# Performance work log

Measured on AMD Instinct MI355X. Metric: run time of the kernel, lower is better.

Reference implementation:

```python
import jax, jax.numpy as jnp
import numpy as np

N = 100000
E = 1600000
F_IN, H, C = 128, 128, 64


def setup_inputs() -> dict:
    key = jax.random.key(0)
    ks = jax.random.split(key, 8)
    x = jax.random.normal(ks[0], (N, F_IN), dtype=jnp.float32)
    edge_index = jax.random.randint(ks[1], (2, E), 0, N, dtype=jnp.int64)
    s = lambda fi: (1.0 / np.sqrt(fi))
    # SAGEConv1: lin_l (applied to mean-aggregated neighbors, has bias), lin_r (root, no bias)
    W1l = jax.random.uniform(ks[2], (H, F_IN), jnp.float32, -s(F_IN), s(F_IN))
    b1 = jnp.zeros((H,), jnp.float32)
    W1r = jax.random.uniform(ks[3], (H, F_IN), jnp.float32, -s(F_IN), s(F_IN))
    # SAGEConv2
    W2l = jax.random.uniform(ks[4], (C, H), jnp.float32, -s(H), s(H))
    b2 = jnp.zeros((C,), jnp.float32)
    W2r = jax.random.uniform(ks[5], (C, H), jnp.float32, -s(H), s(H))
    return {"x": x, "edge_index": edge_index, "W1l": W1l, "b1": b1, "W1r": W1r,
            "W2l": W2l, "b2": b2, "W2r": W2r}


def _mean_aggr(x, src, dst):
    # mean over incoming neighbors (PyG flow: edge_index[0]=source -> edge_index[1]=target)
    msg = x[src]                                            # [E, F] big gather
    summed = jax.ops.segment_sum(msg, dst, num_segments=N)  # [N, F]
    cnt = jax.ops.segment_sum(jnp.ones((src.shape[0],), x.dtype), dst, num_segments=N)
    return summed / jnp.clip(cnt, 1.0)[:, None]


def _sage_conv(x, src, dst, Wl, b, Wr):
    agg = _mean_aggr(x, src, dst)
    return agg @ Wl.T + b + x @ Wr.T


def _iconv(x, src, dst):
    # weight-free GCN propagation: D^-1/2 (A + I) D^-1/2 @ x
    loops = jnp.arange(N, dtype=src.dtype)
    s2 = jnp.concatenate([src, loops])
    d2 = jnp.concatenate([dst, loops])
    deg = jax.ops.segment_sum(jnp.ones((s2.shape[0],), x.dtype), d2, num_segments=N)
    dis = jnp.where(deg > 0, jax.lax.rsqrt(jnp.maximum(deg, 1.0)), 0.0)
    norm = dis[s2] * dis[d2]                               # [E+N]
    return jax.ops.segment_sum(norm[:, None] * x[s2], d2, num_segments=N)


def reference(x, edge_index, W1l, b1, W1r, W2l, b2, W2r):
    src, dst = edge_index[0], edge_index[1]
    h = jax.nn.relu(_sage_conv(x, src, dst, W1l, b1, W1r))
    # F.dropout(training=False) -> identity in eval mode
    h = _sage_conv(h, src, dst, W2l, b2, W2r)
    return _iconv(h, src, dst)
```

## Files before the change

kernel.cpp:

```cpp
#include <hip/hip_runtime.h>

#define GN 100000
#define GE 1600000
#define GF 128
#define GH 128
#define GC 64

#define NB 392
#define SLABSZ 5376
#define P1_EDGES 4096
#define P1_BLOCKS ((GE + P1_EDGES - 1) / P1_EDGES)
#define CASTX_BLOCKS 12500

typedef __attribute__((ext_vector_type(8))) short v8s;
typedef __attribute__((ext_vector_type(4))) float v4f;

__device__ __forceinline__ unsigned short f2bf(float f) {
    union { float f; unsigned u; } a; a.f = f;
    unsigned r = a.u + 0x7fff + ((a.u >> 16) & 1);
    return (unsigned short)(r >> 16);
}
__device__ __forceinline__ float bf2f(unsigned short b) {
    union { unsigned u; float f; } a; a.u = ((unsigned)b) << 16;
    return a.f;
}

__global__ __launch_bounds__(256) void prep_kernel(
    unsigned* __restrict__ slab, int* __restrict__ bucket_cnt,
    const int* __restrict__ src, const int* __restrict__ dst,
    unsigned short* __restrict__ xb, const float* __restrict__ x,
    unsigned short* w1l, unsigned short* w1r,
    unsigned short* w2l, unsigned short* w2r,
    const float* W1l, const float* W1r,
    const float* W2l, const float* W2r)
{
    __shared__ int hist[512];
    __shared__ int scanex[512];
    __shared__ int cursor[512];
    __shared__ int gbase[512];
    __shared__ int ssum[256];
    __shared__ unsigned stage[P1_EDGES];
    __shared__ unsigned short sbid[P1_EDGES];

    int tid = threadIdx.x;
    int blk = blockIdx.x;

    if (blk >= P1_BLOCKS) {
        int cb = blk - P1_BLOCKS;
        if (cb < CASTX_BLOCKS) {
            int i = cb * 256 + tid;
            float4 v = ((const float4*)x)[i];
            ushort4 u;
            u.x = f2bf(v.x); u.y = f2bf(v.y); u.z = f2bf(v.z); u.w = f2bf(v.w);
            ((ushort4*)xb)[i] = u;
            return;
        }
        int i = (cb - CASTX_BLOCKS) * 256 + tid;
        const float* s; unsigned short* d; int off;
        if      (i <  4096) { s = W1l; d = w1l; off = i; }
        else if (i <  8192) { s = W1r; d = w1r; off = i - 4096; }
        else if (i < 10240) { s = W2l; d = w2l; off = i - 8192; }
        else if (i < 12288) { s = W2r; d = w2r; off = i - 10240; }
        else return;
        float4 v = ((const float4*)s)[off];
        ushort4 u;
        u.x = f2bf(v.x); u.y = f2bf(v.y); u.z = f2bf(v.z); u.w = f2bf(v.w);
        ((ushort4*)d)[off] = u;
        return;
    }

    int e0 = blk * P1_EDGES;
    int nE = min(P1_EDGES, GE - e0);

    unsigned pk[16]; int bk[16];
    hist[tid] = 0; hist[tid + 256] = 0;
    __syncthreads();
    #pragma unroll
    for (int j = 0; j < 16; ++j) {
        int i = j * 256 + tid;
        if (i < nE) {
            int e = e0 + i;
            int d = dst[e], s = src[e];
            int b = d >> 8;
            pk[j] = ((unsigned)(d & 255) << 17) | (unsigned)s;
            bk[j] = b;
            atomicAdd(&hist[b], 1);
        } else bk[j] = -1;
    }
    __syncthreads();
    int a0 = hist[2 * tid], a1 = hist[2 * tid + 1];
    int s2 = a0 + a1;
    ssum[tid] = s2;
    __syncthreads();
    for (int off = 1; off < 256; off <<= 1) {
        int v = (tid >= off) ? ssum[tid - off] : 0;
        __syncthreads();
        ssum[tid] += v;
        __syncthreads();
    }
    int pbase = ssum[tid] - s2;
    scanex[2 * tid] = pbase;          cursor[2 * tid] = pbase;
    scanex[2 * tid + 1] = pbase + a0; cursor[2 * tid + 1] = pbase + a0;
    __syncthreads();
    #pragma unroll
    for (int j = 0; j < 16; ++j) {
        if (bk[j] >= 0) {
            int pos = atomicAdd(&cursor[bk[j]], 1);
            stage[pos] = pk[j];
            sbid[pos] = (unsigned short)bk[j];
        }
    }
    for (int b = tid; b < NB; b += 256) {
        int c = hist[b];
        gbase[b] = c ? atomicAdd(&bucket_cnt[b], c) : 0;
    }
    __syncthreads();
    for (int i = tid; i < nE; i += 256) {
        int b = sbid[i];
        int go = gbase[b] + (i - scanex[b]);
        if (go < SLABSZ)
            slab[(size_t)b * SLABSZ + go] = stage[i];
    }
}

__global__ __launch_bounds__(256) void bucket_pass2_kernel(
    int* __restrict__ csr, int* __restrict__ row_ptr,
    float* __restrict__ invc, float* __restrict__ dis,
    const unsigned* __restrict__ slab, const int* __restrict__ bucket_cnt)
{
    __shared__ int deg_l[256];
    __shared__ int excl[256];
    __shared__ int cur[256];
    __shared__ int ssum[256];
    __shared__ int bstart_s;
    __shared__ unsigned stage[SLABSZ];

    int t = threadIdx.x;
    int b = blockIdx.x;

    int c0 = (2 * t < NB) ? bucket_cnt[2 * t] : 0;
    int c1 = (2 * t + 1 < NB) ? bucket_cnt[2 * t + 1] : 0;
    int sc = c0 + c1;
    ssum[t] = sc;
    __syncthreads();
    for (int off = 1; off < 256; off <<= 1) {
        int v = (t >= off) ? ssum[t - off] : 0;
        __syncthreads();
        ssum[t] += v;
        __syncthreads();
    }
    int pb = ssum[t] - sc;
    if (2 * t == b)     bstart_s = pb;
    if (2 * t + 1 == b) bstart_s = pb + c0;
    if (b == NB - 1 && t == 0) row_ptr[GN] = GE;

    int cnt = min(bucket_cnt[b], SLABSZ);
    const unsigned* sp = slab + (size_t)b * SLABSZ;
    deg_l[t] = 0;
    __syncthreads();
    int base = bstart_s;
    for (int i = t; i < cnt; i += 256)
        atomicAdd(&deg_l[sp[i] >> 17], 1);
    __syncthreads();
    int dg = deg_l[t];
    ssum[t] = dg;
    __syncthreads();
    for (int off = 1; off < 256; off <<= 1) {
        int v = (t >= off) ? ssum[t - off] : 0;
        __syncthreads();
        ssum[t] += v;
        __syncthreads();
    }
    int ex = ssum[t] - dg;
    excl[t] = ex; cur[t] = ex;
    __syncthreads();
    int d = b * 256 + t;
    if (d < GN) {
        row_ptr[d] = base + ex;
        float c = (float)dg;
        invc[d] = 1.0f / fmaxf(c, 1.0f);
        dis[d] = rsqrtf(c + 1.0f);
    }
    for (int i = t; i < cnt; i += 256) {
        unsigned p = sp[i];
        int pos = atomicAdd(&cur[p >> 17], 1);
        stage[pos] = p & 0x1FFFFu;
    }
    __syncthreads();
    for (int i = t; i < cnt; i += 256)
        csr[base + i] = (int)stage[i];
}

__global__ __launch_bounds__(256) void fused_gemm_kernel(
    unsigned short* __restrict__ P, unsigned short* __restrict__ Q,
    const unsigned short* __restrict__ A1, const unsigned short* __restrict__ A2,
    const unsigned short* __restrict__ W1, const unsigned short* __restrict__ W2,
    const unsigned short* __restrict__ Wl, const unsigned short* __restrict__ Wr,
    const float* __restrict__ b1, const float* __restrict__ b2, int M)
{
    __shared__ unsigned short hs[256][136];

    int tid = threadIdx.x;
    int wv = tid >> 6, lane = tid & 63;
    int lm = lane & 15, quad = lane >> 4;
    int m_base = blockIdx.x * 256 + wv * 64;
    int row_l0 = wv * 64;

    for (int nh = 0; nh < 2; ++nh) {
        int n_base = nh * 64;
        v4f acc[4][4];
        #pragma unroll
        for (int mt = 0; mt < 4; ++mt)
            #pragma unroll
            for (int nt = 0; nt < 4; ++nt) acc[mt][nt] = (v4f){0.f,0.f,0.f,0.f};

        #pragma unroll
        for (int ks = 0; ks < 4; ++ks) {
            int koff = ks * 32 + quad * 8;
            v8s a1[4], a2[4], bw1[4], bw2[4];
            #pragma unroll
            for (int mt = 0; mt < 4; ++mt) {
                int row = m_base + mt * 16 + lm;
                if (row < M) {
                    a1[mt] = *(const v8s*)(A1 + (size_t)row * 128 + koff);
                    a2[mt] = *(const v8s*)(A2 + (size_t)row * 128 + koff);
                } else {
                    a1[mt] = (v8s){0,0,0,0,0,0,0,0};
                    a2[mt] = (v8s){0,0,0,0,0,0,0,0};
                }
            }
            #pragma unroll
            for (int nt = 0; nt < 4; ++nt) {
                int col = n_base + nt * 16 + lm;
                bw1[nt] = *(const v8s*)(W1 + (size_t)col * 128 + koff);
                bw2[nt] = *(const v8s*)(W2 + (size_t)col * 128 + koff);
            }
            #pragma unroll
            for (int mt = 0; mt < 4; ++mt)
                #pragma unroll
                for (int nt = 0; nt < 4; ++nt) {
                    acc[mt][nt] = __builtin_amdgcn_mfma_f32_16x16x32_bf16(a1[mt], bw1[nt], acc[mt][nt], 0, 0, 0);
                    acc[mt][nt] = __builtin_amdgcn_mfma_f32_16x16x32_bf16(a2[mt], bw2[nt], acc[mt][nt], 0, 0, 0);
                }
        }

        #pragma unroll
        for (int mt = 0; mt < 4; ++mt)
            #pragma unroll
            for (int r = 0; r < 4; ++r) {
                int rl = row_l0 + mt * 16 + quad * 4 + r;
                #pragma unroll
                for (int nt = 0; nt < 4; ++nt) {
                    int col = n_base + nt * 16 + lm;
                    float v = acc[mt][nt][r] + b1[col];
                    hs[rl][col] = f2bf(fmaxf(v, 0.f));
                }
            }
    }
    __syncthreads();

    v4f accP[4][4], accQ[4][4];
    #pragma unroll
    for (int mt = 0; mt < 4; ++mt)
        #pragma unroll
        for (int nt = 0; nt < 4; ++nt) {
            accP[mt][nt] = (v4f){0.f,0.f,0.f,0.f};
            accQ[mt][nt] = (v4f){0.f,0.f,0.f,0.f};
        }

    #pragma unroll
    for (int ks = 0; ks < 4; ++ks) {
        int koff = ks * 32 + quad * 8;
        v8s af[4], bl[4], br[4];
        #pragma unroll
        for (int mt = 0; mt < 4; ++mt)
            af[mt] = *(const v8s*)&hs[row_l0 + mt * 16 + lm][koff];
        #pragma unroll
        for (int nt = 0; nt < 4; ++nt) {
            int col = nt * 16 + lm;
            bl[nt] = *(const v8s*)(Wl + (size_t)col * 128 + koff);
            br[nt] = *(const v8s*)(Wr + (size_t)col * 128 + koff);
        }
        #pragma unroll
        for (int mt = 0; mt < 4; ++mt)
            #pragma unroll
            for (int nt = 0; nt < 4; ++nt) {
                accP[mt][nt] = __builtin_amdgcn_mfma_f32_16x16x32_bf16(af[mt], bl[nt], accP[mt][nt], 0, 0, 0);
                accQ[mt][nt] = __builtin_amdgcn_mfma_f32_16x16x32_bf16(af[mt], br[nt], accQ[mt][nt], 0, 0, 0);
            }
    }

    #pragma unroll
    for (int mt = 0; mt < 4; ++mt)
        #pragma unroll
        for (int r = 0; r < 4; ++r) {
            int row = m_base + mt * 16 + quad * 4 + r;
            if (row >= M) continue;
            #pragma unroll
            for (int nt = 0; nt < 4; ++nt) {
                int col = nt * 16 + lm;
                P[(size_t)row * 64 + col] = f2bf(accP[mt][nt][r]);
                Q[(size_t)row * 64 + col] = f2bf(accQ[mt][nt][r] + b2[col]);
            }
        }
}

__global__ __launch_bounds__(256) void gather_mean128_kernel(
    unsigned short* __restrict__ out, const unsigned short* __restrict__ in,
    const float* __restrict__ invc, const int* __restrict__ row_ptr,
    const int* __restrict__ csr, int N)
{
    int wid = (blockIdx.x * 256 + threadIdx.x) >> 6;
    int lane = threadIdx.x & 63;
    if (wid >= N) return;
    int half = lane >> 5, k = lane & 31;
    int beg = row_ptr[wid], end = row_ptr[wid + 1];
    float ax = 0.f, ay = 0.f, az = 0.f, aw = 0.f;
    int j = beg + half;
    for (; j + 6 < end; j += 8) {
        int s0 = csr[j], s1 = csr[j + 2], s2 = csr[j + 4], s3 = csr[j + 6];
        ushort4 a = ((const ushort4*)(in + (size_t)s0 * 128))[k];
        ushort4 b = ((const ushort4*)(in + (size_t)s1 * 128))[k];
        ushort4 c = ((const ushort4*)(in + (size_t)s2 * 128))[k];
        ushort4 d = ((const ushort4*)(in + (size_t)s3 * 128))[k];
        ax += (bf2f(a.x) + bf2f(b.x)) + (bf2f(c.x) + bf2f(d.x));
        ay += (bf2f(a.y) + bf2f(b.y)) + (bf2f(c.y) + bf2f(d.y));
        az += (bf2f(a.z) + bf2f(b.z)) + (bf2f(c.z) + bf2f(d.z));
        aw += (bf2f(a.w) + bf2f(b.w)) + (bf2f(c.w) + bf2f(d.w));
    }
    for (; j < end; j += 2) {
        ushort4 a = ((const ushort4*)(in + (size_t)csr[j] * 128))[k];
        ax += bf2f(a.x); ay += bf2f(a.y); az += bf2f(a.z); aw += bf2f(a.w);
    }
    ax += __shfl_xor(ax, 32); ay += __shfl_xor(ay, 32);
    az += __shfl_xor(az, 32); aw += __shfl_xor(aw, 32);
    if (half == 0) {
        float ic = invc[wid];
        ushort4 o;
        o.x = f2bf(ax * ic); o.y = f2bf(ay * ic);
        o.z = f2bf(az * ic); o.w = f2bf(aw * ic);
        ((ushort4*)(out + (size_t)wid * 128))[k] = o;
    }
}

__global__ __launch_bounds__(256) void gather_combine_kernel(
    unsigned short* __restrict__ h2s, const unsigned short* __restrict__ p,
    const unsigned short* __restrict__ q,
    const float* __restrict__ invc, const float* __restrict__ dis,
    const int* __restrict__ row_ptr, const int* __restrict__ csr, int N)
{
    int wid = (blockIdx.x * 256 + threadIdx.x) >> 6;
    int lane = threadIdx.x & 63;
    if (wid >= N) return;
    int half = lane >> 5, k = lane & 31;
    int beg = row_ptr[wid], end = row_ptr[wid + 1];
    float ax = 0.f, ay = 0.f;
    int j = beg + half;
    for (; j + 6 < end; j += 8) {
        int s0 = csr[j], s1 = csr[j + 2], s2 = csr[j + 4], s3 = csr[j + 6];
        unsigned a = ((const unsigned*)(p + (size_t)s0 * 64))[k];
        unsigned b = ((const unsigned*)(p + (size_t)s1 * 64))[k];
        unsigned c = ((const unsigned*)(p + (size_t)s2 * 64))[k];
        unsigned d = ((const unsigned*)(p + (size_t)s3 * 64))[k];
        ax += (bf2f((unsigned short)(a & 0xffff)) + bf2f((unsigned short)(b & 0xffff)))
            + (bf2f((unsigned short)(c & 0xffff)) + bf2f((unsigned short)(d & 0xffff)));
        ay += (bf2f((unsigned short)(a >> 16)) + bf2f((unsigned short)(b >> 16)))
            + (bf2f((unsigned short)(c >> 16)) + bf2f((unsigned short)(d >> 16)));
    }
    for (; j < end; j += 2) {
        unsigned a = ((const unsigned*)(p + (size_t)csr[j] * 64))[k];
        ax += bf2f((unsigned short)(a & 0xffff));
        ay += bf2f((unsigned short)(a >> 16));
    }
    ax += __shfl_xor(ax, 32); ay += __shfl_xor(ay, 32);
    if (half == 0) {
        float ic = invc[wid], dd = dis[wid];
        unsigned qv = ((const unsigned*)(q + (size_t)wid * 64))[k];
        float ox = dd * (ax * ic + bf2f((unsigned short)(qv & 0xffff)));
        float oy = dd * (ay * ic + bf2f((unsigned short)(qv >> 16)));
        unsigned o = (unsigned)f2bf(ox) | ((unsigned)f2bf(oy) << 16);
        ((unsigned*)(h2s + (size_t)wid * 64))[k] = o;
    }
}

__global__ __launch_bounds__(256) void iconv_kernel(
    float* __restrict__ out, const unsigned short* __restrict__ h2s,
    const float* __restrict__ dis, const int* __restrict__ row_ptr,
    const int* __restrict__ csr, int N)
{
    int wid = (blockIdx.x * 256 + threadIdx.x) >> 6;
    int lane = threadIdx.x & 63;
    if (wid >= N) return;
    int half = lane >> 5, k = lane & 31;
    int beg = row_ptr[wid], end = row_ptr[wid + 1];
    float ax = 0.f, ay = 0.f;
    int j = beg + half;
    for (; j + 6 < end; j += 8) {
        int s0 = csr[j], s1 = csr[j + 2], s2 = csr[j + 4], s3 = csr[j + 6];
        unsigned a = ((const unsigned*)(h2s + (size_t)s0 * 64))[k];
        unsigned b = ((const unsigned*)(h2s + (size_t)s1 * 64))[k];
        unsigned c = ((const unsigned*)(h2s + (size_t)s2 * 64))[k];
        unsigned d = ((const unsigned*)(h2s + (size_t)s3 * 64))[k];
        ax += (bf2f((unsigned short)(a & 0xffff)) + bf2f((unsigned short)(b & 0xffff)))
            + (bf2f((unsigned short)(c & 0xffff)) + bf2f((unsigned short)(d & 0xffff)));
        ay += (bf2f((unsigned short)(a >> 16)) + bf2f((unsigned short)(b >> 16)))
            + (bf2f((unsigned short)(c >> 16)) + bf2f((unsigned short)(d >> 16)));
    }
    for (; j < end; j += 2) {
        unsigned a = ((const unsigned*)(h2s + (size_t)csr[j] * 64))[k];
        ax += bf2f((unsigned short)(a & 0xffff));
        ay += bf2f((unsigned short)(a >> 16));
    }
    ax += __shfl_xor(ax, 32); ay += __shfl_xor(ay, 32);
    if (half == 0) {
        unsigned s = ((const unsigned*)(h2s + (size_t)wid * 64))[k];
        ax += bf2f((unsigned short)(s & 0xffff));
        ay += bf2f((unsigned short)(s >> 16));
        float dd = dis[wid];
        ((float2*)(out + (size_t)wid * 64))[k] = make_float2(dd * ax, dd * ay);
    }
}

extern "C" void kernel_launch(void* const* d_in, const int* in_sizes, int n_in,
                              void* d_out, int out_size, void* d_ws, size_t ws_size,
                              hipStream_t stream) {
    const float* x   = (const float*)d_in[0];
    const int*   ei  = (const int*)d_in[1];
    const float* W1l = (const float*)d_in[2];
    const float* b1  = (const float*)d_in[3];
    const float* W1r = (const float*)d_in[4];
    const float* W2l = (const float*)d_in[5];
    const float* b2  = (const float*)d_in[6];
    const float* W2r = (const float*)d_in[7];
    float* out = (float*)d_out;

    const int* src = ei;
    const int* dst = ei + GE;

    float* invc = (float*)d_ws;
    float* dis  = invc + GN;
    unsigned short* regA = (unsigned short*)(dis + GN);
    unsigned short* regB = regA + (size_t)GN * 128;
    unsigned short* xb    = regA;
    unsigned short* aggx  = regB;
    unsigned short* pb    = regB;
    unsigned short* qb    = regB + (size_t)GN * 64;
    unsigned short* h2s   = regA;
    unsigned short* w1lb = regB + (size_t)GN * 128;
    unsigned short* w1rb = w1lb + GH * GF;
    unsigned short* w2lb = w1rb + GH * GF;
    unsigned short* w2rb = w2lb + GC * GH;
    int* row_ptr      = (int*)(w2rb + GC * GH);
    int* bucket_cnt   = row_ptr + GN + 1;
    unsigned* slab    = (unsigned*)(bucket_cnt + NB);
    int* csr          = (int*)(slab + (size_t)NB * SLABSZ);

    unsigned short* pq = (unsigned short*)(csr + GE);
    pb = pq;
    qb = pq + (size_t)GN * 64;
    h2s = regB;

    const int T = 256;
    const int g_wave = (GN * 64 + T - 1) / T;
    dim3 g_fused((GN + 255) / 256, 1);

    hipMemsetAsync(bucket_cnt, 0, NB * sizeof(int), stream);
    prep_kernel<<<P1_BLOCKS + CASTX_BLOCKS + 48, T, 0, stream>>>(
        slab, bucket_cnt, src, dst,
        xb, x, w1lb, w1rb, w2lb, w2rb, W1l, W1r, W2l, W2r);

    bucket_pass2_kernel<<<NB, T, 0, stream>>>(csr, row_ptr, invc, dis,
                                              slab, bucket_cnt);

    gather_mean128_kernel<<<g_wave, T, 0, stream>>>(aggx, xb, invc, row_ptr, csr, GN);

    fused_gemm_kernel<<<g_fused, T, 0, stream>>>(pb, qb, aggx, xb,
                                                 w1lb, w1rb, w2lb, w2rb,
                                                 b1, b2, GN);

    gather_combine_kernel<<<g_wave, T, 0, stream>>>(h2s, pb, qb, invc, dis,
                                                    row_ptr, csr, GN);

    iconv_kernel<<<g_wave, T, 0, stream>>>(out, h2s, dis, row_ptr, csr, GN);
}
```

Measured before the change: 387.0 us.

## Restructure CSR gathers to full-wave rows with lane-broadcast neighbor indices

After: 345.6 us. -10.7%, faster.

```diff
diff --git a/kernel.cpp b/kernel.cpp
--- a/kernel.cpp
+++ b/kernel.cpp
@@ -313,34 +313,38 @@
     int wid = (blockIdx.x * 256 + threadIdx.x) >> 6;
     int lane = threadIdx.x & 63;
     if (wid >= N) return;
-    int half = lane >> 5, k = lane & 31;
-    int beg = row_ptr[wid], end = row_ptr[wid + 1];
-    float ax = 0.f, ay = 0.f, az = 0.f, aw = 0.f;
-    int j = beg + half;
-    for (; j + 6 < end; j += 8) {
-        int s0 = csr[j], s1 = csr[j + 2], s2 = csr[j + 4], s3 = csr[j + 6];
-        ushort4 a = ((const ushort4*)(in + (size_t)s0 * 128))[k];
-        ushort4 b = ((const ushort4*)(in + (size_t)s1 * 128))[k];
-        ushort4 c = ((const ushort4*)(in + (size_t)s2 * 128))[k];
-        ushort4 d = ((const ushort4*)(in + (size_t)s3 * 128))[k];
-        ax += (bf2f(a.x) + bf2f(b.x)) + (bf2f(c.x) + bf2f(d.x));
-        ay += (bf2f(a.y) + bf2f(b.y)) + (bf2f(c.y) + bf2f(d.y));
-        az += (bf2f(a.z) + bf2f(b.z)) + (bf2f(c.z) + bf2f(d.z));
-        aw += (bf2f(a.w) + bf2f(b.w)) + (bf2f(c.w) + bf2f(d.w));
-    }
-    for (; j < end; j += 2) {
-        ushort4 a = ((const ushort4*)(in + (size_t)csr[j] * 128))[k];
-        ax += bf2f(a.x); ay += bf2f(a.y); az += bf2f(a.z); aw += bf2f(a.w);
-    }
-    ax += __shfl_xor(ax, 32); ay += __shfl_xor(ay, 32);
-    az += __shfl_xor(az, 32); aw += __shfl_xor(aw, 32);
-    if (half == 0) {
-        float ic = invc[wid];
-        ushort4 o;
-        o.x = f2bf(ax * ic); o.y = f2bf(ay * ic);
-        o.z = f2bf(az * ic); o.w = f2bf(aw * ic);
-        ((ushort4*)(out + (size_t)wid * 128))[k] = o;
-    }
+    int beg = __builtin_amdgcn_readfirstlane(row_ptr[wid]);
+    int end = __builtin_amdgcn_readfirstlane(row_ptr[wid + 1]);
+    int d = end - beg;
+    float a0 = 0.f, a1 = 0.f;
+    if (d > 0) {
+        int dc = min(d, 64);
+        int idx = csr[beg + ((lane < dc) ? lane : (dc - 1))];
+        for (int t = 0; t < dc; t += 16) {
+            unsigned v[16];
+            #pragma unroll
+            for (int u = 0; u < 16; ++u) {
+                int tt = t + u;
+                int s = __builtin_amdgcn_readlane(idx, (tt < dc) ? tt : (dc - 1));
+                unsigned x = ((const unsigned*)(in + (size_t)s * 128))[lane];
+                v[u] = (tt < dc) ? x : 0u;
+            }
+            #pragma unroll
+            for (int u = 0; u < 16; ++u) {
+                a0 += bf2f((unsigned short)(v[u] & 0xffff));
+                a1 += bf2f((unsigned short)(v[u] >> 16));
+            }
+        }
+        for (int j = beg + 64; j < end; ++j) {
+            int s = __builtin_amdgcn_readfirstlane(csr[j]);
+            unsigned x = ((const unsigned*)(in + (size_t)s * 128))[lane];
+            a0 += bf2f((unsigned short)(x & 0xffff));
+            a1 += bf2f((unsigned short)(x >> 16));
+        }
+    }
+    float ic = invc[wid];
+    unsigned o = (unsigned)f2bf(a0 * ic) | ((unsigned)f2bf(a1 * ic) << 16);
+    ((unsigned*)(out + (size_t)wid * 128))[lane] = o;
 }
 
 __global__ __launch_bounds__(256) void gather_combine_kernel(
@@ -352,35 +356,33 @@
     int wid = (blockIdx.x * 256 + threadIdx.x) >> 6;
     int lane = threadIdx.x & 63;
     if (wid >= N) return;
-    int half = lane >> 5, k = lane & 31;
-    int beg = row_ptr[wid], end = row_ptr[wid + 1];
-    float ax = 0.f, ay = 0.f;
-    int j = beg + half;
-    for (; j + 6 < end; j += 8) {
-        int s0 = csr[j], s1 = csr[j + 2], s2 = csr[j + 4], s3 = csr[j + 6];
-        unsigned a = ((const unsigned*)(p + (size_t)s0 * 64))[k];
-        unsigned b = ((const unsigned*)(p + (size_t)s1 * 64))[k];
-        unsigned c = ((const unsigned*)(p + (size_t)s2 * 64))[k];
-        unsigned d = ((const unsigned*)(p + (size_t)s3 * 64))[k];
-        ax += (bf2f((unsigned short)(a & 0xffff)) + bf2f((unsigned short)(b & 0xffff)))
-            + (bf2f((unsigned short)(c & 0xffff)) + bf2f((unsigned short)(d & 0xffff)));
-        ay += (bf2f((unsigned short)(a >> 16)) + bf2f((unsigned short)(b >> 16)))
-            + (bf2f((unsigned short)(c >> 16)) + bf2f((unsigned short)(d >> 16)));
-    }
-    for (; j < end; j += 2) {
-        unsigned a = ((const unsigned*)(p + (size_t)csr[j] * 64))[k];
-        ax += bf2f((unsigned short)(a & 0xffff));
-        ay += bf2f((unsigned short)(a >> 16));
-    }
-    ax += __shfl_xor(ax, 32); ay += __shfl_xor(ay, 32);
-    if (half == 0) {
-        float ic = invc[wid], dd = dis[wid];
-        unsigned qv = ((const unsigned*)(q + (size_t)wid * 64))[k];
-        float ox = dd * (ax * ic + bf2f((unsigned short)(qv & 0xffff)));
-        float oy = dd * (ay * ic + bf2f((unsigned short)(qv >> 16)));
-        unsigned o = (unsigned)f2bf(ox) | ((unsigned)f2bf(oy) << 16);
-        ((unsigned*)(h2s + (size_t)wid * 64))[k] = o;
-    }
+    int beg = __builtin_amdgcn_readfirstlane(row_ptr[wid]);
+    int end = __builtin_amdgcn_readfirstlane(row_ptr[wid + 1]);
+    int d = end - beg;
+    float a = 0.f;
+    if (d > 0) {
+        int dc = min(d, 64);
+        int idx = csr[beg + ((lane < dc) ? lane : (dc - 1))];
+        for (int t = 0; t < dc; t += 16) {
+            unsigned short v[16];
+            #pragma unroll
+            for (int u = 0; u < 16; ++u) {
+                int tt = t + u;
+                int s = __builtin_amdgcn_readlane(idx, (tt < dc) ? tt : (dc - 1));
+                unsigned short x = p[(size_t)s * 64 + lane];
+                v[u] = (tt < dc) ? x : (unsigned short)0;
+            }
+            #pragma unroll
+            for (int u = 0; u < 16; ++u) a += bf2f(v[u]);
+        }
+        for (int j = beg + 64; j < end; ++j) {
+            int s = __builtin_amdgcn_readfirstlane(csr[j]);
+            a += bf2f(p[(size_t)s * 64 + lane]);
+        }
+    }
+    float ic = invc[wid], dd = dis[wid];
+    float qv = bf2f(q[(size_t)wid * 64 + lane]);
+    h2s[(size_t)wid * 64 + lane] = f2bf(dd * (a * ic + qv));
 }
 
 __global__ __launch_bounds__(256) void iconv_kernel(
@@ -391,34 +393,32 @@
     int wid = (blockIdx.x * 256 + threadIdx.x) >> 6;
     int lane = threadIdx.x & 63;
     if (wid >= N) return;
-    int half = lane >> 5, k = lane & 31;
-    int beg = row_ptr[wid], end = row_ptr[wid + 1];
-    float ax = 0.f, ay = 0.f;
-    int j = beg + half;
-    for (; j + 6 < end; j += 8) {
-        int s0 = csr[j], s1 = csr[j + 2], s2 = csr[j + 4], s3 = csr[j + 6];
-        unsigned a = ((const unsigned*)(h2s + (size_t)s0 * 64))[k];
-        unsigned b = ((const unsigned*)(h2s + (size_t)s1 * 64))[k];
-        unsigned c = ((const unsigned*)(h2s + (size_t)s2 * 64))[k];
-        unsigned d = ((const unsigned*)(h2s + (size_t)s3 * 64))[k];
-        ax += (bf2f((unsigned short)(a & 0xffff)) + bf2f((unsigned short)(b & 0xffff)))
-            + (bf2f((unsigned short)(c & 0xffff)) + bf2f((unsigned short)(d & 0xffff)));
-        ay += (bf2f((unsigned short)(a >> 16)) + bf2f((unsigned short)(b >> 16)))
-            + (bf2f((unsigned short)(c >> 16)) + bf2f((unsigned short)(d >> 16)));
-    }
-    for (; j < end; j += 2) {
-        unsigned a = ((const unsigned*)(h2s + (size_t)csr[j] * 64))[k];
-        ax += bf2f((unsigned short)(a & 0xffff));
-        ay += bf2f((unsigned short)(a >> 16));
-    }
-    ax += __shfl_xor(ax, 32); ay += __shfl_xor(ay, 32);
-    if (half == 0) {
-        unsigned s = ((const unsigned*)(h2s + (size_t)wid * 64))[k];
-        ax += bf2f((unsigned short)(s & 0xffff));
-        ay += bf2f((unsigned short)(s >> 16));
-        float dd = dis[wid];
-        ((float2*)(out + (size_t)wid * 64))[k] = make_float2(dd * ax, dd * ay);
-    }
+    int beg = __builtin_amdgcn_readfirstlane(row_ptr[wid]);
+    int end = __builtin_amdgcn_readfirstlane(row_ptr[wid + 1]);
+    int d = end - beg;
+    float a = 0.f;
+    if (d > 0) {
+        int dc = min(d, 64);
+        int idx = csr[beg + ((lane < dc) ? lane : (dc - 1))];
+        for (int t = 0; t < dc; t += 16) {
+            unsigned short v[16];
+            #pragma unroll
+            for (int u = 0; u < 16; ++u) {
+                int tt = t + u;
+                int s = __builtin_amdgcn_readlane(idx, (tt < dc) ? tt : (dc - 1));
+                unsigned short x = h2s[(size_t)s * 64 + lane];
+                v[u] = (tt < dc) ? x : (unsigned short)0;
+            }
+            #pragma unroll
+            for (int u = 0; u < 16; ++u) a += bf2f(v[u]);
+        }
+        for (int j = beg + 64; j < end; ++j) {
+            int s = __builtin_amdgcn_readfirstlane(csr[j]);
+            a += bf2f(h2s[(size_t)s * 64 + lane]);
+        }
+    }
+    a += bf2f(h2s[(size_t)wid * 64 + lane]);
+    out[(size_t)wid * 64 + lane] = dis[wid] * a;
 }
 
 extern "C" void kernel_launch(void* const* d_in, const int* in_sizes, int n_in,
@@ -443,9 +443,6 @@
     unsigned short* regB = regA + (size_t)GN * 128;
     unsigned short* xb    = regA;
     unsigned short* aggx  = regB;
-    unsigned short* pb    = regB;
-    unsigned short* qb    = regB + (size_t)GN * 64;
-    unsigned short* h2s   = regA;
     unsigned short* w1lb = regB + (size_t)GN * 128;
     unsigned short* w1rb = w1lb + GH * GF;
     unsigned short* w2lb = w1rb + GH * GF;
@@ -454,11 +451,10 @@
     int* bucket_cnt   = row_ptr + GN + 1;
     unsigned* slab    = (unsigned*)(bucket_cnt + NB);
     int* csr          = (int*)(slab + (size_t)NB * SLABSZ);
-
     unsigned short* pq = (unsigned short*)(csr + GE);
-    pb = pq;
-    qb = pq + (size_t)GN * 64;
-    h2s = regB;
+    unsigned short* pb = pq;
+    unsigned short* qb = pq + (size_t)GN * 64;
+    unsigned short* h2s = regB;
 
     const int T = 256;
     const int g_wave = (GN * 64 + T - 1) / T;
```
